# Kernel optimization log

Hardware: AMD Instinct MI355X
Metric: run time of the kernel (lower is better)

## Reference

```python
import jax, jax.numpy as jnp
import numpy as np

NH = 8        # num_heads
KS = 64       # key_size
C_IN = 256
C_OUT = 3 * NH * KS   # 1536
GROUPS = 3 * NH       # 24
EPS = 1e-5
H = W = 64


def setup_inputs() -> dict:
    key = jax.random.key(0)
    k1, k2 = jax.random.split(key)
    x = jax.random.normal(k1, (1, C_IN, H, W), dtype=jnp.float32)
    conv_w = jax.random.normal(k2, (C_OUT, C_IN, 1, 1), dtype=jnp.float32) * 0.05
    gn_w = jnp.ones((C_OUT,), dtype=jnp.float32)
    gn_b = jnp.zeros((C_OUT,), dtype=jnp.float32)
    return {"x": x, "conv_w": conv_w, "gn_w": gn_w, "gn_b": gn_b}


def reference(x, conv_w, gn_w, gn_b):
    B, _, h, w = x.shape
    # 1x1 conv (normalize=True -> no bias): per-pixel GEMM over channels
    attn = jnp.einsum('bchw,oc->bohw', x, conv_w[:, :, 0, 0])  # [B, 1536, H, W]
    # GroupNorm: 24 groups of KS channels, normalized over (KS, H, W)
    g = attn.reshape(B, GROUPS, -1)
    mean = g.mean(axis=-1, keepdims=True)
    var = g.var(axis=-1, keepdims=True)
    g = (g - mean) * jax.lax.rsqrt(var + EPS)
    attn = g.reshape(B, C_OUT, h, w) * gn_w[None, :, None, None] + gn_b[None, :, None, None]
    # split into key, query, value (in that order, per chunk(3, dim=2))
    attn = attn.reshape(B, NH, 3 * KS, h * w)
    key_, query, value = jnp.split(attn, 3, axis=2)   # each [B, NH, KS, HW]
    # saliency = q^T @ k / sqrt(KS) -> [B, NH, HW, HW]
    saliency = jnp.einsum('bnkq,bnkl->bnql', query, key_) / jnp.sqrt(jnp.float32(KS))
    mask = jax.nn.softmax(saliency, axis=-1)
    # out = v @ mask^T -> [B, NH, KS, HW]
    out = jnp.einsum('bnkl,bnql->bnkq', value, mask)
    return out.reshape(B, NH * KS, h, w)
```

## Files before the change

kernel.cpp:

```cpp
#include <hip/hip_runtime.h>

typedef __bf16 bf16;
typedef __bf16 bf16x8 __attribute__((ext_vector_type(8)));
typedef __bf16 bf16x4 __attribute__((ext_vector_type(4)));
typedef float f32x4 __attribute__((ext_vector_type(4)));
typedef float f32x16 __attribute__((ext_vector_type(16)));


#define QF 0.18033688011112042f
#define EXPF(x) __builtin_amdgcn_exp2f(x)

union U4 { bf16x4 v; unsigned u[2]; };
union U8 { bf16x8 v; unsigned u[4]; };

__global__ void k_misc(const float* __restrict__ x, const float* __restrict__ w,
                       bf16* __restrict__ xT, bf16* __restrict__ wb, float* __restrict__ cs) {
    int b = blockIdx.x;
    if (b < 512) {
        int t = b * 256 + threadIdx.x;
        int p  = t & 4095;
        int c0 = (t >> 12) * 8;
        bf16x8 o;
#pragma unroll
        for (int j = 0; j < 8; j++) o[j] = (bf16)x[(c0 + j) * 4096 + p];
        *(bf16x8*)(xT + p * 256 + c0) = o;
    } else if (b < 896) {
        int idx = ((b - 512) * 256 + threadIdx.x) * 4;
        float4 f = *(const float4*)(w + idx);
        bf16x4 o;
        o[0] = (bf16)f.x; o[1] = (bf16)f.y; o[2] = (bf16)f.z; o[3] = (bf16)f.w;
        *(bf16x4*)(wb + idx) = o;
    } else {
#pragma unroll
        for (int i = 0; i < 12; i++) cs[i * 256 + threadIdx.x] = 0.f;
    }
}

__global__ __launch_bounds__(256) void k_conv(const bf16* __restrict__ Wb,
                                              const bf16* __restrict__ xT,
                                              bf16* __restrict__ qkvT,
                                              float* __restrict__ cs) {
    __shared__ __attribute__((aligned(16))) bf16 xs[64 * 72];
    __shared__ __attribute__((aligned(16))) bf16 ws2[64 * 72];
    int wid = threadIdx.x >> 6, lane = threadIdx.x & 63;
    int quad = lane >> 4, l15 = lane & 15;
    int g  = blockIdx.x % 24;
    int pb = (blockIdx.x / 24) * 64;
    int h = g / 3, sec = g % 3;
    int ob = g * 64;

    int srow = threadIdx.x >> 2;
    int scol = (threadIdx.x & 3) * 16;

    f32x4 acc[4];
#pragma unroll
    for (int c = 0; c < 4; c++) acc[c] = (f32x4){0.f, 0.f, 0.f, 0.f};

    bf16x8 fx0 = *(const bf16x8*)(xT + (pb + srow) * 256 + scol);
    bf16x8 fx1 = *(const bf16x8*)(xT + (pb + srow) * 256 + scol + 8);
    bf16x8 fw0 = *(const bf16x8*)(Wb + (ob + srow) * 256 + scol);
    bf16x8 fw1 = *(const bf16x8*)(Wb + (ob + srow) * 256 + scol + 8);

    for (int c4 = 0; c4 < 4; c4++) {
        __syncthreads();
        *(bf16x8*)(xs  + srow * 72 + scol)     = fx0;
        *(bf16x8*)(xs  + srow * 72 + scol + 8) = fx1;
        *(bf16x8*)(ws2 + srow * 72 + scol)     = fw0;
        *(bf16x8*)(ws2 + srow * 72 + scol + 8) = fw1;
        __syncthreads();

        if (c4 < 3) {
            int co = (c4 + 1) * 64;
            fx0 = *(const bf16x8*)(xT + (pb + srow) * 256 + co + scol);
            fx1 = *(const bf16x8*)(xT + (pb + srow) * 256 + co + scol + 8);
            fw0 = *(const bf16x8*)(Wb + (ob + srow) * 256 + co + scol);
            fw1 = *(const bf16x8*)(Wb + (ob + srow) * 256 + co + scol + 8);
        }

#pragma unroll
        for (int k2 = 0; k2 < 2; k2++) {
            bf16x8 a = *(const bf16x8*)(ws2 + (wid * 16 + l15) * 72 + k2 * 32 + quad * 8);
#pragma unroll
            for (int c = 0; c < 4; c++) {
                bf16x8 b = *(const bf16x8*)(xs + (c * 16 + l15) * 72 + k2 * 32 + quad * 8);
                acc[c] = __builtin_amdgcn_mfma_f32_16x16x32_bf16(a, b, acc[c], 0, 0, 0);
            }
        }
    }

    int ch0 = wid * 16 + quad * 4;
#pragma unroll
    for (int r = 0; r < 4; r++) {
        float sp  = acc[0][r] + acc[1][r] + acc[2][r] + acc[3][r];
        float ssp = acc[0][r] * acc[0][r] + acc[1][r] * acc[1][r]
                  + acc[2][r] * acc[2][r] + acc[3][r] * acc[3][r];
#pragma unroll
        for (int m = 1; m < 16; m <<= 1) {
            sp  += __shfl_xor(sp,  m, 64);
            ssp += __shfl_xor(ssp, m, 64);
        }
        if (l15 == 0) {
            atomicAdd(cs + (ob + ch0 + r) * 2,     sp);
            atomicAdd(cs + (ob + ch0 + r) * 2 + 1, ssp);
        }
    }

    __syncthreads();
    bf16* tile = xs;
    if (sec == 2) {
#pragma unroll
        for (int c = 0; c < 4; c++)
#pragma unroll
            for (int r = 0; r < 4; r++)
                tile[(ch0 + r) * 72 + c * 16 + l15] = (bf16)acc[c][r];
    } else {
#pragma unroll
        for (int c = 0; c < 4; c++) {
            bf16x4 o;
#pragma unroll
            for (int r = 0; r < 4; r++) o[r] = (bf16)acc[c][r];
            *(bf16x4*)(&tile[(c * 16 + l15) * 72 + ch0]) = o;
        }
    }
    __syncthreads();
    bf16* base = qkvT + h * 786432;
    int t = threadIdx.x;
    if (sec == 2) {
        bf16* V = base + 524288;
#pragma unroll
        for (int it = 0; it < 2; it++) {
            int e = it * 256 + t; int ch = e >> 3; int pxo = (e & 7) * 8;
            *(bf16x8*)(V + ch * 4096 + pb + pxo) = *(const bf16x8*)(&tile[ch * 72 + pxo]);
        }
    } else {
        bf16* dst = base + (sec == 0 ? 262144 : 0);
#pragma unroll
        for (int it = 0; it < 2; it++) {
            int e = it * 256 + t; int px = e >> 3; int cho = (e & 7) * 8;
            *(bf16x8*)(dst + (pb + px) * 64 + cho) = *(const bf16x8*)(&tile[px * 72 + cho]);
        }
    }
}

__global__ __launch_bounds__(256) void k_normqk(bf16* __restrict__ qkv,
                                                const float2* __restrict__ cs,
                                                const float* __restrict__ gnw,
                                                const float* __restrict__ gnb) {
    int h    = blockIdx.x >> 8;
    int base = (blockIdx.x & 255) * 2048;
    int isQ  = base < 262144;
    int g    = h * 3 + (isQ ? 1 : 0);

    int c = threadIdx.x & 63;
    float2 v = cs[g * 64 + c];
    float s = v.x, ss = v.y;
#pragma unroll
    for (int m = 1; m < 64; m <<= 1) { s += __shfl_xor(s, m, 64); ss += __shfl_xor(ss, m, 64); }
    const float N = 262144.0f;
    float mean = s / N;
    float inv  = rsqrtf(ss / N - mean * mean + 1e-5f);
    float f = isQ ? QF : 1.0f;

    int e = base + threadIdx.x * 8;
    int gc = h * 192 + (isQ ? 64 : 0) + (e & 63);
    bf16* p = qkv + h * 786432 + e;
    bf16x8 vv = *(bf16x8*)p;
    bf16x8 o;
#pragma unroll
    for (int j = 0; j < 8; j++) {
        float gw = gnw[gc + j];
        float a = inv * gw * f;
        float b = (gnb[gc + j] - mean * inv * gw) * f;
        o[j] = (bf16)(a * (float)vv[j] + b);
    }
    *(bf16x8*)p = o;
}

#define PF_BLOCK(S, PFA, PFB)                                                   \
    {                                                                           \
        float p0 = EXPF(S[0]),  p1 = EXPF(S[1]),  p2 = EXPF(S[2]),  p3 = EXPF(S[3]);   \
        float p4 = EXPF(S[4]),  p5 = EXPF(S[5]),  p6 = EXPF(S[6]),  p7 = EXPF(S[7]);   \
        float p8 = EXPF(S[8]),  p9 = EXPF(S[9]),  p10 = EXPF(S[10]), p11 = EXPF(S[11]); \
        float p12 = EXPF(S[12]), p13 = EXPF(S[13]), p14 = EXPF(S[14]), p15 = EXPF(S[15]); \
        lacc += (((p0 + p1) + (p2 + p3)) + ((p4 + p5) + (p6 + p7)))             \
              + (((p8 + p9) + (p10 + p11)) + ((p12 + p13) + (p14 + p15)));      \
        U4 lo, hi;                                                              \
        lo.v[0] = (bf16)p0;  lo.v[1] = (bf16)p1;  lo.v[2] = (bf16)p2;  lo.v[3] = (bf16)p3;  \
        hi.v[0] = (bf16)p4;  hi.v[1] = (bf16)p5;  hi.v[2] = (bf16)p6;  hi.v[3] = (bf16)p7;  \
        unsigned sa = half ? lo.u[0] : hi.u[0];                                 \
        unsigned sb = half ? lo.u[1] : hi.u[1];                                 \
        unsigned ra = (unsigned)__shfl_xor((int)sa, 32, 64);                    \
        unsigned rb = (unsigned)__shfl_xor((int)sb, 32, 64);                    \
        U8 fA;                                                                  \
        fA.u[0] = half ? ra : lo.u[0];  fA.u[1] = half ? rb : lo.u[1];          \
        fA.u[2] = half ? hi.u[0] : ra;  fA.u[3] = half ? hi.u[1] : rb;          \
        PFA = fA.v;                                                             \
        U4 lo2, hi2;                                                            \
        lo2.v[0] = (bf16)p8;  lo2.v[1] = (bf16)p9;  lo2.v[2] = (bf16)p10; lo2.v[3] = (bf16)p11; \
        hi2.v[0] = (bf16)p12; hi2.v[1] = (bf16)p13; hi2.v[2] = (bf16)p14; hi2.v[3] = (bf16)p15; \
        unsigned sc = half ? lo2.u[0] : hi2.u[0];                               \
        unsigned sd = half ? lo2.u[1] : hi2.u[1];                               \
        unsigned rc = (unsigned)__shfl_xor((int)sc, 32, 64);                    \
        unsigned rd = (unsigned)__shfl_xor((int)sd, 32, 64);                    \
        U8 fB;                                                                  \
        fB.u[0] = half ? rc : lo2.u[0];  fB.u[1] = half ? rd : lo2.u[1];        \
        fB.u[2] = half ? hi2.u[0] : rc;  fB.u[3] = half ? hi2.u[1] : rd;        \
        PFB = fB.v;                                                             \
    }

__global__ __launch_bounds__(256, 4) void k_attn(const bf16* __restrict__ qkvT,
                                                 bf16* __restrict__ Opart,
                                                 float* __restrict__ Lsum) {
    int bid   = blockIdx.x;
    int h     = bid & 7;
    int qb    = (bid >> 3) & 31;
    int split = bid >> 8;
    int wid = threadIdx.x >> 6, lane = threadIdx.x & 63;
    int l31 = lane & 31, half = lane >> 5;
    const bf16* QT = qkvT + h * 786432;
    const bf16* KT = QT + 262144;
    const bf16* V  = QT + 524288;
    int qw = qb * 128 + wid * 32;

    __shared__ __attribute__((aligned(16))) bf16 Ks[64 * 72];
    __shared__ __attribute__((aligned(16))) bf16 Vs[64 * 72];

    int r0   = threadIdx.x >> 3;
    int koff = (threadIdx.x & 7) * 8;

    bf16x8 bq[4];
#pragma unroll
    for (int ks = 0; ks < 4; ks++)
        bq[ks] = *(const bf16x8*)(QT + (qw + l31) * 64 + ks * 16 + half * 8);

    f32x16 oacc0 = (f32x16)(0.0f), oacc1 = (f32x16)(0.0f);
    float ls = 0.f;

    int t0 = split * 16, t1 = t0 + 16;

    bf16x8 kf0, kf1, vf0, vf1;
    {
        int lb0 = t0 * 64;
        kf0 = *(const bf16x8*)(KT + (lb0 + r0) * 64 + koff);
        kf1 = *(const bf16x8*)(KT + (lb0 + r0 + 32) * 64 + koff);
        vf0 = *(const bf16x8*)(V + r0 * 4096 + lb0 + koff);
        vf1 = *(const bf16x8*)(V + (r0 + 32) * 4096 + lb0 + koff);
    }

    for (int lt = t0; lt < t1; lt++) {
        __syncthreads();
        *(bf16x8*)(Ks + r0 * 72 + koff)        = kf0;
        *(bf16x8*)(Ks + (r0 + 32) * 72 + koff) = kf1;
        *(bf16x8*)(Vs + r0 * 72 + koff)        = vf0;
        *(bf16x8*)(Vs + (r0 + 32) * 72 + koff) = vf1;
        __syncthreads();

        if (lt + 1 < t1) {
            int nb = (lt + 1) * 64;
            kf0 = *(const bf16x8*)(KT + (nb + r0) * 64 + koff);
            kf1 = *(const bf16x8*)(KT + (nb + r0 + 32) * 64 + koff);
            vf0 = *(const bf16x8*)(V + r0 * 4096 + nb + koff);
            vf1 = *(const bf16x8*)(V + (r0 + 32) * 4096 + nb + koff);
        }

        f32x16 s0 = (f32x16)(0.0f), s1 = (f32x16)(0.0f);
#pragma unroll
        for (int ks = 0; ks < 4; ks++) {
            s0 = __builtin_amdgcn_mfma_f32_32x32x16_bf16(
                *(const bf16x8*)(Ks + l31 * 72 + ks * 16 + half * 8), bq[ks], s0, 0, 0, 0);
            s1 = __builtin_amdgcn_mfma_f32_32x32x16_bf16(
                *(const bf16x8*)(Ks + (32 + l31) * 72 + ks * 16 + half * 8), bq[ks], s1, 0, 0, 0);
        }

        float lacc = ls;
        bf16x8 pf0, pf1, pf2, pf3;
        PF_BLOCK(s0, pf0, pf1);
        PF_BLOCK(s1, pf2, pf3);
        ls = lacc;

        oacc0 = __builtin_amdgcn_mfma_f32_32x32x16_bf16(
            *(const bf16x8*)(Vs + l31 * 72 +  0 + half * 8), pf0, oacc0, 0, 0, 0);
        oacc1 = __builtin_amdgcn_mfma_f32_32x32x16_bf16(
            *(const bf16x8*)(Vs + (32 + l31) * 72 +  0 + half * 8), pf0, oacc1, 0, 0, 0);
        oacc0 = __builtin_amdgcn_mfma_f32_32x32x16_bf16(
            *(const bf16x8*)(Vs + l31 * 72 + 16 + half * 8), pf1, oacc0, 0, 0, 0);
        oacc1 = __builtin_amdgcn_mfma_f32_32x32x16_bf16(
            *(const bf16x8*)(Vs + (32 + l31) * 72 + 16 + half * 8), pf1, oacc1, 0, 0, 0);
        oacc0 = __builtin_amdgcn_mfma_f32_32x32x16_bf16(
            *(const bf16x8*)(Vs + l31 * 72 + 32 + half * 8), pf2, oacc0, 0, 0, 0);
        oacc1 = __builtin_amdgcn_mfma_f32_32x32x16_bf16(
            *(const bf16x8*)(Vs + (32 + l31) * 72 + 32 + half * 8), pf2, oacc1, 0, 0, 0);
        oacc0 = __builtin_amdgcn_mfma_f32_32x32x16_bf16(
            *(const bf16x8*)(Vs + l31 * 72 + 48 + half * 8), pf3, oacc0, 0, 0, 0);
        oacc1 = __builtin_amdgcn_mfma_f32_32x32x16_bf16(
            *(const bf16x8*)(Vs + (32 + l31) * 72 + 48 + half * 8), pf3, oacc1, 0, 0, 0);
    }

    ls += __shfl_xor(ls, 32, 64);
    if (half == 0)
        Lsum[split * 32768 + h * 4096 + qw + l31] = ls;

    bf16* Ob = Opart + split * 2097152;
#pragma unroll
    for (int r = 0; r < 16; r++) {
        int kd = (r & 3) + 8 * (r >> 2) + 4 * half;
        Ob[(h * 64 + kd) * 4096 + qw + l31]        = (bf16)oacc0[r];
        Ob[(h * 64 + 32 + kd) * 4096 + qw + l31]   = (bf16)oacc1[r];
    }
}

__global__ void k_final(const bf16* __restrict__ Opart, const float* __restrict__ Lsum,
                        const float2* __restrict__ cs, const float* __restrict__ gnw,
                        const float* __restrict__ gnb, float* __restrict__ out) {
    int gid = blockIdx.x * 256 + threadIdx.x;
    int row = gid >> 9;
    int c8  = (gid & 511) << 3;
    int h   = row >> 6;

    int g = h * 3 + 2;
    int c = threadIdx.x & 63;
    float2 v = cs[g * 64 + c];
    float s = v.x, ss = v.y;
#pragma unroll
    for (int m = 1; m < 64; m <<= 1) { s += __shfl_xor(s, m, 64); ss += __shfl_xor(ss, m, 64); }
    const float N = 262144.0f;
    float mean = s / N;
    float inv  = rsqrtf(ss / N - mean * mean + 1e-5f);
    int gi = h * 192 + 128 + (row & 63);
    float gw = gnw[gi];
    float va = inv * gw;
    float vb = gnb[gi] - mean * inv * gw;

    float o[8] = {0, 0, 0, 0, 0, 0, 0, 0};
    float l[8] = {0, 0, 0, 0, 0, 0, 0, 0};
#pragma unroll
    for (int sp = 0; sp < 4; sp++) {
        bf16x8 vv = *(const bf16x8*)(Opart + sp * 2097152 + row * 4096 + c8);
        const float* L = Lsum + sp * 32768 + h * 4096 + c8;
        float4 l0 = *(const float4*)L;
        float4 l1 = *(const float4*)(L + 4);
#pragma unroll
        for (int j = 0; j < 8; j++) o[j] += (float)vv[j];
        l[0] += l0.x; l[1] += l0.y; l[2] += l0.z; l[3] += l0.w;
        l[4] += l1.x; l[5] += l1.y; l[6] += l1.z; l[7] += l1.w;
    }
    float4 r0, r1;
    r0.x = va * o[0] / l[0] + vb; r0.y = va * o[1] / l[1] + vb;
    r0.z = va * o[2] / l[2] + vb; r0.w = va * o[3] / l[3] + vb;
    r1.x = va * o[4] / l[4] + vb; r1.y = va * o[5] / l[5] + vb;
    r1.z = va * o[6] / l[6] + vb; r1.w = va * o[7] / l[7] + vb;
    *(float4*)(out + row * 4096 + c8)     = r0;
    *(float4*)(out + row * 4096 + c8 + 4) = r1;
}

extern "C" void kernel_launch(void* const* d_in, const int* in_sizes, int n_in,
                              void* d_out, int out_size, void* d_ws, size_t ws_size,
                              hipStream_t stream) {
    const float* x      = (const float*)d_in[0];
    const float* conv_w = (const float*)d_in[1];
    const float* gn_w   = (const float*)d_in[2];
    const float* gn_b   = (const float*)d_in[3];
    float* out = (float*)d_out;
    char* ws = (char*)d_ws;

    bf16*   qkvT  = (bf16*) (ws);
    bf16*   Opart = (bf16*) (ws + 12582912);
    bf16*   Wb    = (bf16*) (ws + 12582912);
    bf16*   xT    = (bf16*) (ws + 13369344);
    float*  Lsum  = (float*)(ws + 29360128);
    float*  cs    = (float*)(ws + 29884416);

    hipLaunchKernelGGL(k_misc,   dim3(897),  dim3(256), 0, stream, x, conv_w, xT, Wb, cs);
    hipLaunchKernelGGL(k_conv,   dim3(1536), dim3(256), 0, stream, Wb, xT, qkvT, cs);
    hipLaunchKernelGGL(k_normqk, dim3(2048), dim3(256), 0, stream, qkvT, (const float2*)cs, gn_w, gn_b);
    hipLaunchKernelGGL(k_attn,   dim3(1024), dim3(256), 0, stream, qkvT, Opart, Lsum);
    hipLaunchKernelGGL(k_final,  dim3(1024), dim3(256), 0, stream, Opart, Lsum, (const float2*)cs, gn_w, gn_b, out);
}
```

Baseline: 138.5 us.

## Fuse Q/K group-norm into attention kernel, double-buffer LDS, use permlane32 swap

Removes the separate k_normqk pass and instead applies the GroupNorm affine to Q fragments at load time and to K tiles before they are written to LDS inside the attention kernel. K/V shared tiles become double-buffered, which removes the leading barrier per iteration. The P-fragment half-exchange now uses v_permlane32_swap instead of ds shuffles plus selects, and s_setprio is raised around the MFMA blocks. In exchange, each attention block recomputes group statistics and per-element K normalization, which adds VALU work and LDS footprint per block.

Result: slower. 144.5 us (+4.3%).

```diff
diff --git a/kernel.cpp b/kernel.cpp
--- a/kernel.cpp
+++ b/kernel.cpp
@@ -142,40 +142,6 @@
     }
 }
 
-__global__ __launch_bounds__(256) void k_normqk(bf16* __restrict__ qkv,
-                                                const float2* __restrict__ cs,
-                                                const float* __restrict__ gnw,
-                                                const float* __restrict__ gnb) {
-    int h    = blockIdx.x >> 8;
-    int base = (blockIdx.x & 255) * 2048;
-    int isQ  = base < 262144;
-    int g    = h * 3 + (isQ ? 1 : 0);
-
-    int c = threadIdx.x & 63;
-    float2 v = cs[g * 64 + c];
-    float s = v.x, ss = v.y;
-#pragma unroll
-    for (int m = 1; m < 64; m <<= 1) { s += __shfl_xor(s, m, 64); ss += __shfl_xor(ss, m, 64); }
-    const float N = 262144.0f;
-    float mean = s / N;
-    float inv  = rsqrtf(ss / N - mean * mean + 1e-5f);
-    float f = isQ ? QF : 1.0f;
-
-    int e = base + threadIdx.x * 8;
-    int gc = h * 192 + (isQ ? 64 : 0) + (e & 63);
-    bf16* p = qkv + h * 786432 + e;
-    bf16x8 vv = *(bf16x8*)p;
-    bf16x8 o;
-#pragma unroll
-    for (int j = 0; j < 8; j++) {
-        float gw = gnw[gc + j];
-        float a = inv * gw * f;
-        float b = (gnb[gc + j] - mean * inv * gw) * f;
-        o[j] = (bf16)(a * (float)vv[j] + b);
-    }
-    *(bf16x8*)p = o;
-}
-
 #define PF_BLOCK(S, PFA, PFB)                                                   \
     {                                                                           \
         float p0 = EXPF(S[0]),  p1 = EXPF(S[1]),  p2 = EXPF(S[2]),  p3 = EXPF(S[3]);   \
@@ -187,28 +153,25 @@
         U4 lo, hi;                                                              \
         lo.v[0] = (bf16)p0;  lo.v[1] = (bf16)p1;  lo.v[2] = (bf16)p2;  lo.v[3] = (bf16)p3;  \
         hi.v[0] = (bf16)p4;  hi.v[1] = (bf16)p5;  hi.v[2] = (bf16)p6;  hi.v[3] = (bf16)p7;  \
-        unsigned sa = half ? lo.u[0] : hi.u[0];                                 \
-        unsigned sb = half ? lo.u[1] : hi.u[1];                                 \
-        unsigned ra = (unsigned)__shfl_xor((int)sa, 32, 64);                    \
-        unsigned rb = (unsigned)__shfl_xor((int)sb, 32, 64);                    \
-        U8 fA;                                                                  \
-        fA.u[0] = half ? ra : lo.u[0];  fA.u[1] = half ? rb : lo.u[1];          \
-        fA.u[2] = half ? hi.u[0] : ra;  fA.u[3] = half ? hi.u[1] : rb;          \
+        unsigned a0 = lo.u[0], b0 = hi.u[0], a1 = lo.u[1], b1 = hi.u[1];        \
+        asm("v_permlane32_swap_b32 %0, %1" : "+v"(a0), "+v"(b0));               \
+        asm("v_permlane32_swap_b32 %0, %1" : "+v"(a1), "+v"(b1));               \
+        U8 fA; fA.u[0] = a0; fA.u[1] = a1; fA.u[2] = b0; fA.u[3] = b1;          \
         PFA = fA.v;                                                             \
         U4 lo2, hi2;                                                            \
         lo2.v[0] = (bf16)p8;  lo2.v[1] = (bf16)p9;  lo2.v[2] = (bf16)p10; lo2.v[3] = (bf16)p11; \
         hi2.v[0] = (bf16)p12; hi2.v[1] = (bf16)p13; hi2.v[2] = (bf16)p14; hi2.v[3] = (bf16)p15; \
-        unsigned sc = half ? lo2.u[0] : hi2.u[0];                               \
-        unsigned sd = half ? lo2.u[1] : hi2.u[1];                               \
-        unsigned rc = (unsigned)__shfl_xor((int)sc, 32, 64);                    \
-        unsigned rd = (unsigned)__shfl_xor((int)sd, 32, 64);                    \
-        U8 fB;                                                                  \
-        fB.u[0] = half ? rc : lo2.u[0];  fB.u[1] = half ? rd : lo2.u[1];        \
-        fB.u[2] = half ? hi2.u[0] : rc;  fB.u[3] = half ? hi2.u[1] : rd;        \
+        unsigned a2 = lo2.u[0], b2 = hi2.u[0], a3 = lo2.u[1], b3 = hi2.u[1];    \
+        asm("v_permlane32_swap_b32 %0, %1" : "+v"(a2), "+v"(b2));               \
+        asm("v_permlane32_swap_b32 %0, %1" : "+v"(a3), "+v"(b3));               \
+        U8 fB; fB.u[0] = a2; fB.u[1] = a3; fB.u[2] = b2; fB.u[3] = b3;          \
         PFB = fB.v;                                                             \
     }
 
 __global__ __launch_bounds__(256, 4) void k_attn(const bf16* __restrict__ qkvT,
+                                                 const float2* __restrict__ cs,
+                                                 const float* __restrict__ gnw,
+                                                 const float* __restrict__ gnb,
                                                  bf16* __restrict__ Opart,
                                                  float* __restrict__ Lsum) {
     int bid   = blockIdx.x;
@@ -222,16 +185,45 @@
     const bf16* V  = QT + 524288;
     int qw = qb * 128 + wid * 32;
 
-    __shared__ __attribute__((aligned(16))) bf16 Ks[64 * 72];
-    __shared__ __attribute__((aligned(16))) bf16 Vs[64 * 72];
+    __shared__ __attribute__((aligned(16))) bf16 Ks[2][64 * 72];
+    __shared__ __attribute__((aligned(16))) bf16 Vs[2][64 * 72];
 
     int r0   = threadIdx.x >> 3;
     int koff = (threadIdx.x & 7) * 8;
 
+    float2 vK = cs[(h * 3) * 64 + lane];
+    float2 vQ = cs[(h * 3 + 1) * 64 + lane];
+    float sK = vK.x, qK = vK.y, sQ = vQ.x, qQ = vQ.y;
+#pragma unroll
+    for (int m = 1; m < 64; m <<= 1) {
+        sK += __shfl_xor(sK, m, 64); qK += __shfl_xor(qK, m, 64);
+        sQ += __shfl_xor(sQ, m, 64); qQ += __shfl_xor(qQ, m, 64);
+    }
+    const float N = 262144.0f;
+    float meanK = sK / N, invK = rsqrtf(qK / N - meanK * meanK + 1e-5f);
+    float meanQ = sQ / N, invQ = rsqrtf(qQ / N - meanQ * meanQ + 1e-5f);
+
+    float aK[8], bK[8];
+#pragma unroll
+    for (int j = 0; j < 8; j++) {
+        float gw = gnw[h * 192 + koff + j] * invK;
+        aK[j] = gw;
+        bK[j] = gnb[h * 192 + koff + j] - meanK * gw;
+    }
+
     bf16x8 bq[4];
 #pragma unroll
-    for (int ks = 0; ks < 4; ks++)
-        bq[ks] = *(const bf16x8*)(QT + (qw + l31) * 64 + ks * 16 + half * 8);
+    for (int ks = 0; ks < 4; ks++) {
+        bf16x8 raw = *(const bf16x8*)(QT + (qw + l31) * 64 + ks * 16 + half * 8);
+#pragma unroll
+        for (int j = 0; j < 8; j++) {
+            int c = ks * 16 + half * 8 + j;
+            float gw = gnw[h * 192 + 64 + c] * invQ;
+            float av = gw * QF;
+            float bv = (gnb[h * 192 + 64 + c] - meanQ * gw) * QF;
+            bq[ks][j] = (bf16)(av * (float)raw[j] + bv);
+        }
+    }
 
     f32x16 oacc0 = (f32x16)(0.0f), oacc1 = (f32x16)(0.0f);
     float ls = 0.f;
@@ -248,11 +240,18 @@
     }
 
     for (int lt = t0; lt < t1; lt++) {
-        __syncthreads();
-        *(bf16x8*)(Ks + r0 * 72 + koff)        = kf0;
-        *(bf16x8*)(Ks + (r0 + 32) * 72 + koff) = kf1;
-        *(bf16x8*)(Vs + r0 * 72 + koff)        = vf0;
-        *(bf16x8*)(Vs + (r0 + 32) * 72 + koff) = vf1;
+        bf16* ksb = Ks[lt & 1];
+        bf16* vsb = Vs[lt & 1];
+
+        bf16x8 nk0, nk1;
+#pragma unroll
+        for (int j = 0; j < 8; j++) nk0[j] = (bf16)(aK[j] * (float)kf0[j] + bK[j]);
+#pragma unroll
+        for (int j = 0; j < 8; j++) nk1[j] = (bf16)(aK[j] * (float)kf1[j] + bK[j]);
+        *(bf16x8*)(ksb + r0 * 72 + koff)        = nk0;
+        *(bf16x8*)(ksb + (r0 + 32) * 72 + koff) = nk1;
+        *(bf16x8*)(vsb + r0 * 72 + koff)        = vf0;
+        *(bf16x8*)(vsb + (r0 + 32) * 72 + koff) = vf1;
         __syncthreads();
 
         if (lt + 1 < t1) {
@@ -263,14 +262,18 @@
             vf1 = *(const bf16x8*)(V + (r0 + 32) * 4096 + nb + koff);
         }
 
+        const bf16* ka = ksb + l31 * 72 + half * 8;
+        const bf16* kb = ksb + (32 + l31) * 72 + half * 8;
         f32x16 s0 = (f32x16)(0.0f), s1 = (f32x16)(0.0f);
+        __builtin_amdgcn_s_setprio(1);
 #pragma unroll
         for (int ks = 0; ks < 4; ks++) {
             s0 = __builtin_amdgcn_mfma_f32_32x32x16_bf16(
-                *(const bf16x8*)(Ks + l31 * 72 + ks * 16 + half * 8), bq[ks], s0, 0, 0, 0);
+                *(const bf16x8*)(ka + ks * 16), bq[ks], s0, 0, 0, 0);
             s1 = __builtin_amdgcn_mfma_f32_32x32x16_bf16(
-                *(const bf16x8*)(Ks + (32 + l31) * 72 + ks * 16 + half * 8), bq[ks], s1, 0, 0, 0);
-        }
+                *(const bf16x8*)(kb + ks * 16), bq[ks], s1, 0, 0, 0);
+        }
+        __builtin_amdgcn_s_setprio(0);
 
         float lacc = ls;
         bf16x8 pf0, pf1, pf2, pf3;
@@ -278,22 +281,18 @@
         PF_BLOCK(s1, pf2, pf3);
         ls = lacc;
 
-        oacc0 = __builtin_amdgcn_mfma_f32_32x32x16_bf16(
-            *(const bf16x8*)(Vs + l31 * 72 +  0 + half * 8), pf0, oacc0, 0, 0, 0);
-        oacc1 = __builtin_amdgcn_mfma_f32_32x32x16_bf16(
-            *(const bf16x8*)(Vs + (32 + l31) * 72 +  0 + half * 8), pf0, oacc1, 0, 0, 0);
-        oacc0 = __builtin_amdgcn_mfma_f32_32x32x16_bf16(
-            *(const bf16x8*)(Vs + l31 * 72 + 16 + half * 8), pf1, oacc0, 0, 0, 0);
-        oacc1 = __builtin_amdgcn_mfma_f32_32x32x16_bf16(
-            *(const bf16x8*)(Vs + (32 + l31) * 72 + 16 + half * 8), pf1, oacc1, 0, 0, 0);
-        oacc0 = __builtin_amdgcn_mfma_f32_32x32x16_bf16(
-            *(const bf16x8*)(Vs + l31 * 72 + 32 + half * 8), pf2, oacc0, 0, 0, 0);
-        oacc1 = __builtin_amdgcn_mfma_f32_32x32x16_bf16(
-            *(const bf16x8*)(Vs + (32 + l31) * 72 + 32 + half * 8), pf2, oacc1, 0, 0, 0);
-        oacc0 = __builtin_amdgcn_mfma_f32_32x32x16_bf16(
-            *(const bf16x8*)(Vs + l31 * 72 + 48 + half * 8), pf3, oacc0, 0, 0, 0);
-        oacc1 = __builtin_amdgcn_mfma_f32_32x32x16_bf16(
-            *(const bf16x8*)(Vs + (32 + l31) * 72 + 48 + half * 8), pf3, oacc1, 0, 0, 0);
+        const bf16* va = vsb + l31 * 72 + half * 8;
+        const bf16* vb = vsb + (32 + l31) * 72 + half * 8;
+        __builtin_amdgcn_s_setprio(1);
+        oacc0 = __builtin_amdgcn_mfma_f32_32x32x16_bf16(*(const bf16x8*)(va +  0), pf0, oacc0, 0, 0, 0);
+        oacc1 = __builtin_amdgcn_mfma_f32_32x32x16_bf16(*(const bf16x8*)(vb +  0), pf0, oacc1, 0, 0, 0);
+        oacc0 = __builtin_amdgcn_mfma_f32_32x32x16_bf16(*(const bf16x8*)(va + 16), pf1, oacc0, 0, 0, 0);
+        oacc1 = __builtin_amdgcn_mfma_f32_32x32x16_bf16(*(const bf16x8*)(vb + 16), pf1, oacc1, 0, 0, 0);
+        oacc0 = __builtin_amdgcn_mfma_f32_32x32x16_bf16(*(const bf16x8*)(va + 32), pf2, oacc0, 0, 0, 0);
+        oacc1 = __builtin_amdgcn_mfma_f32_32x32x16_bf16(*(const bf16x8*)(vb + 32), pf2, oacc1, 0, 0, 0);
+        oacc0 = __builtin_amdgcn_mfma_f32_32x32x16_bf16(*(const bf16x8*)(va + 48), pf3, oacc0, 0, 0, 0);
+        oacc1 = __builtin_amdgcn_mfma_f32_32x32x16_bf16(*(const bf16x8*)(vb + 48), pf3, oacc1, 0, 0, 0);
+        __builtin_amdgcn_s_setprio(0);
     }
 
     ls += __shfl_xor(ls, 32, 64);
@@ -370,9 +369,9 @@
     float*  Lsum  = (float*)(ws + 29360128);
     float*  cs    = (float*)(ws + 29884416);
 
-    hipLaunchKernelGGL(k_misc,   dim3(897),  dim3(256), 0, stream, x, conv_w, xT, Wb, cs);
-    hipLaunchKernelGGL(k_conv,   dim3(1536), dim3(256), 0, stream, Wb, xT, qkvT, cs);
-    hipLaunchKernelGGL(k_normqk, dim3(2048), dim3(256), 0, stream, qkvT, (const float2*)cs, gn_w, gn_b);
-    hipLaunchKernelGGL(k_attn,   dim3(1024), dim3(256), 0, stream, qkvT, Opart, Lsum);
-    hipLaunchKernelGGL(k_final,  dim3(1024), dim3(256), 0, stream, Opart, Lsum, (const float2*)cs, gn_w, gn_b, out);
-}
+    hipLaunchKernelGGL(k_misc,  dim3(897),  dim3(256), 0, stream, x, conv_w, xT, Wb, cs);
+    hipLaunchKernelGGL(k_conv,  dim3(1536), dim3(256), 0, stream, Wb, xT, qkvT, cs);
+    hipLaunchKernelGGL(k_attn,  dim3(1024), dim3(256), 0, stream, qkvT, (const float2*)cs,
+                       gn_w, gn_b, Opart, Lsum);
+    hipLaunchKernelGGL(k_final, dim3(1024), dim3(256), 0, stream, Opart, Lsum, (const float2*)cs, gn_w, gn_b, out);
+}
```
